# Kernel optimization log

Hardware: AMD Instinct MI355X
Metric: run time of the kernel (lower is better)

Reference implementation:

```python
import jax, jax.numpy as jnp
import numpy as np

N_NODES = 100_000
N_EDGES = 3_200_000
IN_CH = 128
HID = 64


def setup_inputs() -> dict:
    key = jax.random.key(0)
    k0, k1, k2, k3 = jax.random.split(key, 4)
    x = jax.random.normal(k0, (N_NODES, IN_CH), dtype=jnp.float32)
    edge_index = jax.random.randint(k1, (2, N_EDGES), 0, N_NODES)
    # GCNConv internal linear (no bias) -> W1; separate additive bias b1
    W1 = jax.random.normal(k2, (HID, IN_CH), dtype=jnp.float32) * 0.05
    b1 = jnp.zeros((HID,), dtype=jnp.float32)
    W2 = jax.random.normal(k3, (1, HID), dtype=jnp.float32) * 0.05
    b2 = jnp.zeros((1,), dtype=jnp.float32)
    return {"x": x, "edge_index": edge_index, "W1": W1, "b1": b1, "W2": W2, "b2": b2}


def reference(x, edge_index, W1, b1, W2, b2):
    n = x.shape[0]
    # --- GCNConv: add self-loops, symmetric degree normalization ---
    loops = jnp.arange(n, dtype=edge_index.dtype)
    src = jnp.concatenate([edge_index[0], loops])  # [E+N]
    dst = jnp.concatenate([edge_index[1], loops])  # [E+N]
    deg = jax.ops.segment_sum(jnp.ones_like(dst, dtype=x.dtype), dst, num_segments=n)
    dinv = jnp.where(deg > 0, jax.lax.rsqrt(deg), 0.0)
    norm = dinv[src] * dinv[dst]                   # [E+N]
    h = x @ W1.T                                   # [N, HID]
    msg = h[src] * norm[:, None]                   # [E+N, HID] gather
    agg = jax.ops.segment_sum(msg, dst, num_segments=n) + b1  # scatter-add
    # --- ReLU + Linear(hidden, 1) + squeeze ---
    out = jax.nn.relu(agg) @ W2.T + b2             # [N, 1]
    return out.squeeze(-1)
```

## Files before the change

kernel.cpp:

```cpp
#include <hip/hip_runtime.h>


typedef unsigned int u32;
typedef unsigned short u16;
typedef __attribute__((ext_vector_type(8))) short bf16x8;
typedef __attribute__((ext_vector_type(4))) float f32x4;

#define PK 8192
#define EPT (PK/256)
#define CAPB 9216

__device__ __forceinline__ u16 f2bf(float f) {
    u32 b = __float_as_uint(f);
    b += 0x7FFF + ((b >> 16) & 1);
    return (u16)(b >> 16);
}
__device__ __forceinline__ float bf2f(u16 u) {
    return __uint_as_float(((u32)u) << 16);
}
__device__ __forceinline__ bf16x8 pack8(float4 lo, float4 hi) {
    bf16x8 o;
    o[0] = (short)f2bf(lo.x); o[1] = (short)f2bf(lo.y);
    o[2] = (short)f2bf(lo.z); o[3] = (short)f2bf(lo.w);
    o[4] = (short)f2bf(hi.x); o[5] = (short)f2bf(hi.y);
    o[6] = (short)f2bf(hi.z); o[7] = (short)f2bf(hi.w);
    return o;
}

__global__ __launch_bounds__(512) void init_kernel(int* __restrict__ bcur, int NB) {
    int t = threadIdx.x;
    if (t < NB) bcur[t] = t * CAPB;
}

__global__ __launch_bounds__(256) void wcvt_kernel(const float* __restrict__ W1,
                                                   u16* __restrict__ wbf) {
    int t = threadIdx.x;
#pragma unroll
    for (int i = 0; i < 32; ++i) wbf[i * 256 + t] = f2bf(W1[i * 256 + t]);
}

__global__ __launch_bounds__(256) void part_kernel(const int* __restrict__ src,
                                                   const int* __restrict__ dst,
                                                   int* __restrict__ bcur,
                                                   u32* __restrict__ ebuf, int E, int NB) {
    __shared__ u32 stage[PK];
    __shared__ u16 sbid[PK];
    __shared__ int h[512], loff[512], gbase[512], cur[512];
    int t = threadIdx.x;
    int e0 = blockIdx.x * PK;
    int e1 = e0 + PK; if (e1 > E) e1 = E;
    int cnt = e1 - e0;
    for (int i = t; i < 512; i += 256) { h[i] = 0; cur[i] = 0; }
    __syncthreads();
    int dreg[EPT];
#pragma unroll
    for (int i = 0; i < EPT; ++i) {
        int e = e0 + i * 256 + t;
        dreg[i] = (e < e1) ? dst[e] : -1;
        if (dreg[i] >= 0) atomicAdd(&h[dreg[i] >> 8], 1);
    }
    __syncthreads();
    if (t < 64) {
        int carry = 0;
        for (int c = 0; c < 8; ++c) {
            int idx = c * 64 + t;
            int v = h[idx], incl = v;
            for (int d2 = 1; d2 < 64; d2 <<= 1) {
                int o = __shfl_up(incl, d2);
                if (t >= d2) incl += o;
            }
            loff[idx] = carry + incl - v;
            carry += __shfl(incl, 63);
        }
    }
    __syncthreads();
    for (int idx = t; idx < NB; idx += 256)
        gbase[idx] = atomicAdd(&bcur[idx], h[idx]);
    __syncthreads();
#pragma unroll
    for (int i = 0; i < EPT; ++i) {
        int d = dreg[i];
        if (d >= 0) {
            int e = e0 + i * 256 + t;
            int s = src[e];
            int bk = d >> 8;
            int r = atomicAdd(&cur[bk], 1);
            int p = loff[bk] + r;
            stage[p] = ((u32)(d & 255) << 17) | (u32)s;
            sbid[p] = (u16)bk;
        }
    }
    __syncthreads();
    for (int i = t; i < cnt; i += 256) {
        int bk = sbid[i];
        ebuf[gbase[bk] + (i - loff[bk])] = stage[i];
    }
}

__global__ __launch_bounds__(512) void bscan2_kernel(const int* __restrict__ bcur,
                                                     int* __restrict__ boff,
                                                     int NB, int E) {
    __shared__ int buf[2][512];
    int t = threadIdx.x;
    int v = (t < NB) ? (bcur[t] - t * CAPB) : 0;
    buf[0][t] = v;
    __syncthreads();
    int pi = 0;
    for (int d = 1; d < 512; d <<= 1) {
        int val = buf[pi][t];
        if (t >= d) val += buf[pi][t - d];
        buf[pi ^ 1][t] = val;
        pi ^= 1;
        __syncthreads();
    }
    if (t < NB) boff[t] = buf[pi][t] - v;
    if (t == 0) boff[NB] = E;
}

__global__ __launch_bounds__(256) void csrb2_kernel(const u32* __restrict__ ebuf,
                                                    const int* __restrict__ boff,
                                                    int* __restrict__ csr,
                                                    int* __restrict__ offs,
                                                    int* __restrict__ degc,
                                                    int N) {
    __shared__ u32 stage[CAPB];
    __shared__ int h2[256], lofs[256], cur2[256];
    int t = threadIdx.x;
    int b = blockIdx.x;
    int base = b << 8;
    int c0 = boff[b];
    int cnt = boff[b + 1] - c0;
    int e0 = b * CAPB;
    h2[t] = 0; cur2[t] = 0;
    __syncthreads();
    for (int e = t; e < cnt; e += 256) atomicAdd(&h2[(int)(ebuf[e0 + e] >> 17)], 1);
    __syncthreads();
    if (t < 64) {
        int carry = 0;
        for (int c = 0; c < 4; ++c) {
            int idx = c * 64 + t;
            int v = h2[idx], incl = v;
            for (int d2 = 1; d2 < 64; d2 <<= 1) {
                int o = __shfl_up(incl, d2);
                if (t >= d2) incl += o;
            }
            lofs[idx] = carry + incl - v;
            carry += __shfl(incl, 63);
        }
    }
    __syncthreads();
    int n = base + t;
    if (n < N) { offs[n] = c0 + lofs[t]; degc[n] = h2[t]; }
    if (cnt <= CAPB) {
        for (int e = t; e < cnt; e += 256) {
            u32 pk = ebuf[e0 + e];
            int dl = (int)(pk >> 17);
            int r = atomicAdd(&cur2[dl], 1);
            stage[lofs[dl] + r] = pk & 0x1FFFF;
        }
        __syncthreads();
        for (int e = t; e < cnt; e += 256) csr[c0 + e] = (int)stage[e];
    } else {
        for (int e = t; e < cnt; e += 256) {
            u32 pk = ebuf[e0 + e];
            int dl = (int)(pk >> 17);
            int r = atomicAdd(&cur2[dl], 1);
            csr[c0 + lofs[dl] + r] = (int)(pk & 0x1FFFF);
        }
    }
}

__global__ __launch_bounds__(256) void gemm_kernel(const float* __restrict__ x,
                                                   const u16* __restrict__ wbf,
                                                   const int* __restrict__ degc,
                                                   u16* __restrict__ gb, int N) {
    int t = threadIdx.x;
    int lane = t & 63;
    int wv = t >> 6;
    int n0 = blockIdx.x * 64 + wv * 16;
    int r = lane & 15;
    int g = lane >> 4;

    int nr = n0 + r; if (nr >= N) nr = N - 1;
    const float* xrow = x + (size_t)nr * 128 + g * 8;
    bf16x8 afr[4];
#pragma unroll
    for (int ks = 0; ks < 4; ++ks) {
        float4 lo = *(const float4*)(xrow + ks * 32);
        float4 hi = *(const float4*)(xrow + ks * 32 + 4);
        afr[ks] = pack8(lo, hi);
    }

    f32x4 acc[4] = {f32x4{0.f,0.f,0.f,0.f}, f32x4{0.f,0.f,0.f,0.f},
                    f32x4{0.f,0.f,0.f,0.f}, f32x4{0.f,0.f,0.f,0.f}};
#pragma unroll
    for (int ct = 0; ct < 4; ++ct) {
        const u16* wrow = wbf + (ct * 16 + r) * 128 + g * 8;
#pragma unroll
        for (int ks = 0; ks < 4; ++ks) {
            bf16x8 bfr = *(const bf16x8*)(wrow + ks * 32);
            acc[ct] = __builtin_amdgcn_mfma_f32_16x16x32_bf16(afr[ks], bfr, acc[ct], 0, 0, 0);
        }
    }

#pragma unroll
    for (int reg = 0; reg < 4; ++reg) {
        int n = n0 + g * 4 + reg;
        if (n < N) {
            float dv = rsqrtf((float)(degc[n] + 1));
#pragma unroll
            for (int ct = 0; ct < 4; ++ct)
                gb[(size_t)n * 64 + ct * 16 + r] = f2bf(dv * acc[ct][reg]);
        }
    }
}

__global__ __launch_bounds__(256) void agg_kernel(const u16* __restrict__ gb,
                                                  const int* __restrict__ csr,
                                                  const int* __restrict__ offs,
                                                  const int* __restrict__ degc,
                                                  const float* __restrict__ W2,
                                                  const float* __restrict__ b1,
                                                  const float* __restrict__ b2,
                                                  float* __restrict__ out, int N) {
    int wid = blockIdx.x * 4 + (threadIdx.x >> 6);
    int lane = threadIdx.x & 63;
    if (wid >= N) return;
    int off = __builtin_amdgcn_readfirstlane(offs[wid]);
    int cnt = __builtin_amdgcn_readfirstlane(degc[wid]);
    const u16* gbl = gb + lane;
    float acc = bf2f(gbl[(size_t)wid * 64]);
    int j = 0;
    for (; j + 16 <= cnt; j += 16) {
        float v[16];
#pragma unroll
        for (int k = 0; k < 16; ++k) {
            int s = csr[off + j + k];
            v[k] = bf2f(gbl[(size_t)s * 64]);
        }
        float s01 = (v[0] + v[1]) + (v[2] + v[3]);
        float s23 = (v[4] + v[5]) + (v[6] + v[7]);
        float s45 = (v[8] + v[9]) + (v[10] + v[11]);
        float s67 = (v[12] + v[13]) + (v[14] + v[15]);
        acc += (s01 + s23) + (s45 + s67);
    }
    for (; j + 4 <= cnt; j += 4) {
        float v[4];
#pragma unroll
        for (int k = 0; k < 4; ++k) {
            int s = csr[off + j + k];
            v[k] = bf2f(gbl[(size_t)s * 64]);
        }
        acc += (v[0] + v[1]) + (v[2] + v[3]);
    }
    for (; j < cnt; ++j) {
        int s = csr[off + j];
        acc += bf2f(gbl[(size_t)s * 64]);
    }
    float dv = rsqrtf((float)(cnt + 1));
    float val = fmaxf(dv * acc + b1[lane], 0.f) * W2[lane];
#pragma unroll
    for (int o = 32; o >= 1; o >>= 1) val += __shfl_xor(val, o);
    if (lane == 0) out[wid] = val + b2[0];
}

extern "C" void kernel_launch(void* const* d_in, const int* in_sizes, int n_in,
                              void* d_out, int out_size, void* d_ws, size_t ws_size,
                              hipStream_t stream) {
    const float* x  = (const float*)d_in[0];
    const int*   ei = (const int*)d_in[1];
    const float* W1 = (const float*)d_in[2];
    const float* b1 = (const float*)d_in[3];
    const float* W2 = (const float*)d_in[4];
    const float* b2 = (const float*)d_in[5];
    float* out = (float*)d_out;

    int N = in_sizes[0] / 128;
    int E = in_sizes[1] / 2;
    const int* src = ei;
    const int* dst = ei + E;
    int NB = (N + 255) >> 8;
    int NBLK = (E + PK - 1) / PK;

    char* ws = (char*)d_ws;
    int* bcur = (int*)(ws + 0x000000);
    int* boff = (int*)(ws + 0x004000);
    int* degc = (int*)(ws + 0x010000);
    int* offs = (int*)(ws + 0x080000);
    u16* wbf  = (u16*)(ws + 0x0F0000);
    u32* ebuf = (u32*)(ws + 0x100000);
    u16* gb   = (u16*)(ws + 0x100000);
    int* csr  = (int*)(ws + 0xF00000);

    init_kernel<<<1, 512, 0, stream>>>(bcur, NB);
    wcvt_kernel<<<1, 256, 0, stream>>>(W1, wbf);
    part_kernel<<<NBLK, 256, 0, stream>>>(src, dst, bcur, ebuf, E, NB);
    bscan2_kernel<<<1, 512, 0, stream>>>(bcur, boff, NB, E);
    csrb2_kernel<<<NB, 256, 0, stream>>>(ebuf, boff, csr, offs, degc, N);
    gemm_kernel<<<(N + 63) / 64, 256, 0, stream>>>(x, wbf, degc, gb, N);
    agg_kernel<<<(N + 3) / 4, 256, 0, stream>>>(gb, csr, offs, degc, W2, b1, b2, out, N);
}
```

Measured before the change: 144.6 us.

## Merge setup kernels, shrink partition chunks, widen partition and CSR blocks to 512

```diff
diff --git a/kernel.cpp b/kernel.cpp
--- a/kernel.cpp
+++ b/kernel.cpp
@@ -1,4 +1,5 @@
 #include <hip/hip_runtime.h>
+#include <hip/hip_bf16.h>
 
 
 typedef unsigned int u32;
@@ -6,40 +7,38 @@
 typedef __attribute__((ext_vector_type(8))) short bf16x8;
 typedef __attribute__((ext_vector_type(4))) float f32x4;
 
-#define PK 8192
-#define EPT (PK/256)
+#define PK 4096
+#define PTH 512
+#define EPT (PK/PTH)
 #define CAPB 9216
 
-__device__ __forceinline__ u16 f2bf(float f) {
-    u32 b = __float_as_uint(f);
-    b += 0x7FFF + ((b >> 16) & 1);
-    return (u16)(b >> 16);
+__device__ __forceinline__ short f2bf(float f) {
+    __hip_bfloat16 h = __float2bfloat16(f);
+    return *reinterpret_cast<short*>(&h);
 }
 __device__ __forceinline__ float bf2f(u16 u) {
     return __uint_as_float(((u32)u) << 16);
 }
 __device__ __forceinline__ bf16x8 pack8(float4 lo, float4 hi) {
     bf16x8 o;
-    o[0] = (short)f2bf(lo.x); o[1] = (short)f2bf(lo.y);
-    o[2] = (short)f2bf(lo.z); o[3] = (short)f2bf(lo.w);
-    o[4] = (short)f2bf(hi.x); o[5] = (short)f2bf(hi.y);
-    o[6] = (short)f2bf(hi.z); o[7] = (short)f2bf(hi.w);
+    o[0] = f2bf(lo.x); o[1] = f2bf(lo.y); o[2] = f2bf(lo.z); o[3] = f2bf(lo.w);
+    o[4] = f2bf(hi.x); o[5] = f2bf(hi.y); o[6] = f2bf(hi.z); o[7] = f2bf(hi.w);
     return o;
 }
 
-__global__ __launch_bounds__(512) void init_kernel(int* __restrict__ bcur, int NB) {
-    int t = threadIdx.x;
-    if (t < NB) bcur[t] = t * CAPB;
-}
-
-__global__ __launch_bounds__(256) void wcvt_kernel(const float* __restrict__ W1,
-                                                   u16* __restrict__ wbf) {
-    int t = threadIdx.x;
-#pragma unroll
-    for (int i = 0; i < 32; ++i) wbf[i * 256 + t] = f2bf(W1[i * 256 + t]);
-}
-
-__global__ __launch_bounds__(256) void part_kernel(const int* __restrict__ src,
+__global__ __launch_bounds__(512) void setup_kernel(int* __restrict__ bcur,
+                                                    const float* __restrict__ W1,
+                                                    u16* __restrict__ wbf, int NB) {
+    int t = threadIdx.x;
+    if (blockIdx.x == 0) {
+        if (t < NB) bcur[t] = t * CAPB;
+    } else {
+#pragma unroll
+        for (int i = 0; i < 16; ++i) wbf[i * 512 + t] = (u16)f2bf(W1[i * 512 + t]);
+    }
+}
+
+__global__ __launch_bounds__(PTH) void part_kernel(const int* __restrict__ src,
                                                    const int* __restrict__ dst,
                                                    int* __restrict__ bcur,
                                                    u32* __restrict__ ebuf, int E, int NB) {
@@ -50,12 +49,12 @@
     int e0 = blockIdx.x * PK;
     int e1 = e0 + PK; if (e1 > E) e1 = E;
     int cnt = e1 - e0;
-    for (int i = t; i < 512; i += 256) { h[i] = 0; cur[i] = 0; }
+    h[t] = 0; cur[t] = 0;
     __syncthreads();
     int dreg[EPT];
 #pragma unroll
     for (int i = 0; i < EPT; ++i) {
-        int e = e0 + i * 256 + t;
+        int e = e0 + i * PTH + t;
         dreg[i] = (e < e1) ? dst[e] : -1;
         if (dreg[i] >= 0) atomicAdd(&h[dreg[i] >> 8], 1);
     }
@@ -74,14 +73,13 @@
         }
     }
     __syncthreads();
-    for (int idx = t; idx < NB; idx += 256)
-        gbase[idx] = atomicAdd(&bcur[idx], h[idx]);
+    if (t < NB) gbase[t] = atomicAdd(&bcur[t], h[t]);
     __syncthreads();
 #pragma unroll
     for (int i = 0; i < EPT; ++i) {
         int d = dreg[i];
         if (d >= 0) {
-            int e = e0 + i * 256 + t;
+            int e = e0 + i * PTH + t;
             int s = src[e];
             int bk = d >> 8;
             int r = atomicAdd(&cur[bk], 1);
@@ -91,7 +89,7 @@
         }
     }
     __syncthreads();
-    for (int i = t; i < cnt; i += 256) {
+    for (int i = t; i < cnt; i += PTH) {
         int bk = sbid[i];
         ebuf[gbase[bk] + (i - loff[bk])] = stage[i];
     }
@@ -117,7 +115,7 @@
     if (t == 0) boff[NB] = E;
 }
 
-__global__ __launch_bounds__(256) void csrb2_kernel(const u32* __restrict__ ebuf,
+__global__ __launch_bounds__(512) void csrb2_kernel(const u32* __restrict__ ebuf,
                                                     const int* __restrict__ boff,
                                                     int* __restrict__ csr,
                                                     int* __restrict__ offs,
@@ -131,9 +129,9 @@
     int c0 = boff[b];
     int cnt = boff[b + 1] - c0;
     int e0 = b * CAPB;
-    h2[t] = 0; cur2[t] = 0;
-    __syncthreads();
-    for (int e = t; e < cnt; e += 256) atomicAdd(&h2[(int)(ebuf[e0 + e] >> 17)], 1);
+    if (t < 256) { h2[t] = 0; cur2[t] = 0; }
+    __syncthreads();
+    for (int e = t; e < cnt; e += 512) atomicAdd(&h2[(int)(ebuf[e0 + e] >> 17)], 1);
     __syncthreads();
     if (t < 64) {
         int carry = 0;
@@ -149,19 +147,21 @@
         }
     }
     __syncthreads();
-    int n = base + t;
-    if (n < N) { offs[n] = c0 + lofs[t]; degc[n] = h2[t]; }
+    if (t < 256) {
+        int n = base + t;
+        if (n < N) { offs[n] = c0 + lofs[t]; degc[n] = h2[t]; }
+    }
     if (cnt <= CAPB) {
-        for (int e = t; e < cnt; e += 256) {
+        for (int e = t; e < cnt; e += 512) {
             u32 pk = ebuf[e0 + e];
             int dl = (int)(pk >> 17);
             int r = atomicAdd(&cur2[dl], 1);
             stage[lofs[dl] + r] = pk & 0x1FFFF;
         }
         __syncthreads();
-        for (int e = t; e < cnt; e += 256) csr[c0 + e] = (int)stage[e];
+        for (int e = t; e < cnt; e += 512) csr[c0 + e] = (int)stage[e];
     } else {
-        for (int e = t; e < cnt; e += 256) {
+        for (int e = t; e < cnt; e += 512) {
             u32 pk = ebuf[e0 + e];
             int dl = (int)(pk >> 17);
             int r = atomicAdd(&cur2[dl], 1);
@@ -210,7 +210,7 @@
             float dv = rsqrtf((float)(degc[n] + 1));
 #pragma unroll
             for (int ct = 0; ct < 4; ++ct)
-                gb[(size_t)n * 64 + ct * 16 + r] = f2bf(dv * acc[ct][reg]);
+                gb[(size_t)n * 64 + ct * 16 + r] = (u16)f2bf(dv * acc[ct][reg]);
         }
     }
 }
@@ -292,11 +292,10 @@
     u16* gb   = (u16*)(ws + 0x100000);
     int* csr  = (int*)(ws + 0xF00000);
 
-    init_kernel<<<1, 512, 0, stream>>>(bcur, NB);
-    wcvt_kernel<<<1, 256, 0, stream>>>(W1, wbf);
-    part_kernel<<<NBLK, 256, 0, stream>>>(src, dst, bcur, ebuf, E, NB);
+    setup_kernel<<<2, 512, 0, stream>>>(bcur, W1, wbf, NB);
+    part_kernel<<<NBLK, PTH, 0, stream>>>(src, dst, bcur, ebuf, E, NB);
     bscan2_kernel<<<1, 512, 0, stream>>>(bcur, boff, NB, E);
-    csrb2_kernel<<<NB, 256, 0, stream>>>(ebuf, boff, csr, offs, degc, N);
+    csrb2_kernel<<<NB, 512, 0, stream>>>(ebuf, boff, csr, offs, degc, N);
     gemm_kernel<<<(N + 63) / 64, 256, 0, stream>>>(x, wbf, degc, gb, N);
     agg_kernel<<<(N + 3) / 4, 256, 0, stream>>>(gb, csr, offs, degc, W2, b1, b2, out, N);
 }
```

After: 134.2 us. 7.2% less time.
